# Optimization experiments

Hardware: AMD Instinct MI355X
Metric: run time of the kernel (lower is better)

## Reference

```python
import jax, jax.numpy as jnp
import numpy as np

B, N, FIN, E, OUT, NH = 8, 1024, 128, 128, 128, 8
HD = E // NH  # head_dim = 16


def setup_inputs() -> dict:
    key = jax.random.key(0)
    ks = jax.random.split(key, 8)
    s = 0.05
    H = jax.random.normal(ks[0], (B, N, FIN), jnp.float32)
    # binary adjacency (sparse-ish graph), stored dense float as the module expects
    A = (jax.random.uniform(ks[1], (B, N, N)) < 0.05).astype(jnp.float32)
    W_lin = jax.random.normal(ks[2], (FIN, E), jnp.float32) * s
    b_lin = jnp.zeros((E,), jnp.float32)
    # nn.MultiheadAttention packed in-projection (q,k,v) and out-projection
    W_in = jax.random.normal(ks[3], (E, 3 * E), jnp.float32) * s
    b_in = jnp.zeros((3 * E,), jnp.float32)
    W_out = jax.random.normal(ks[4], (E, E), jnp.float32) * s
    b_out = jnp.zeros((E,), jnp.float32)
    W_fin = jax.random.normal(ks[5], (E, OUT), jnp.float32) * s
    b_fin = jnp.zeros((OUT,), jnp.float32)
    return dict(H=H, A=A, W_lin=W_lin, b_lin=b_lin, W_in=W_in, b_in=b_in,
                W_out=W_out, b_out=b_out, W_fin=W_fin, b_fin=b_fin)


def reference(H, A, W_lin, b_lin, W_in, b_in, W_out, b_out, W_fin, b_fin):
    # input projection: Linear(128, embed_dim)
    Hp = H @ W_lin + b_lin                                   # (B,N,E)
    # adjacency-gated attention weights: bmm -> LeakyReLU(0.2) -> *A -> softmax
    s = jnp.einsum('bnd,bmd->bnm', Hp, Hp)                   # (B,N,N)
    s = jnp.where(s >= 0, s, 0.2 * s)
    attn_w = jax.nn.softmax(s * A, axis=-1)                  # (B,N,N)
    # nn.MultiheadAttention self-attention with float attn_mask (ADDED to scores)
    qkv = Hp @ W_in + b_in                                   # (B,N,3E)
    q, k, v = jnp.split(qkv, 3, axis=-1)
    q = q.reshape(B, N, NH, HD)
    k = k.reshape(B, N, NH, HD)
    v = v.reshape(B, N, NH, HD)
    scores = jnp.einsum('bnhd,bmhd->bhnm', q, k) / np.sqrt(HD).astype(np.float32)
    scores = scores + attn_w[:, None]                        # mask broadcast over heads
    p = jax.nn.softmax(scores, axis=-1)                      # (B,NH,N,N)
    o = jnp.einsum('bhnm,bmhd->bnhd', p, v).reshape(B, N, E)
    o = o @ W_out + b_out                                    # MHA out_proj
    # output linear; dropout is identity in eval mode
    return o @ W_fin + b_fin                                 # (B,N,OUT)
```

## Files before the change

kernel.cpp:

```cpp
#include <hip/hip_runtime.h>
#include <hip/hip_bf16.h>


using u16 = unsigned short;
typedef short bf16x8 __attribute__((ext_vector_type(8)));
typedef float f32x4 __attribute__((ext_vector_type(4)));
typedef _Float16 f16;
typedef _Float16 f16x4 __attribute__((ext_vector_type(4)));

#define MFMA16(a, b, c) __builtin_amdgcn_mfma_f32_16x16x16f16(a, b, c, 0, 0, 0)

__device__ __forceinline__ u16 f2b(float f) {
    unsigned u = __float_as_uint(f);
    return (u16)((u + 0x7fffu + ((u >> 16) & 1u)) >> 16);
}
__device__ __forceinline__ float b2f(u16 u) {
    return __uint_as_float(((unsigned)u) << 16);
}

__global__ void prep_k(const float* __restrict__ Wlin, const float* __restrict__ Win,
                       const float* __restrict__ Wout, const float* __restrict__ Wfin,
                       const float* __restrict__ bout, const float* __restrict__ bfin,
                       const float* __restrict__ Aadj,
                       u16* __restrict__ WlinTb, u16* __restrict__ WinTb,
                       float* __restrict__ WcombT, float* __restrict__ bcomb,
                       float* __restrict__ rowsum, unsigned char* __restrict__ A8) {
    int i = blockIdx.x * 256 + threadIdx.x;
    if (i >= 81920) {
        int j = i - 81920;
        long long base = (long long)j * 8;
        float4 a0 = *(const float4*)&Aadj[base];
        float4 a1 = *(const float4*)&Aadj[base + 4];
        unsigned long long m = 0;
        m |= (unsigned long long)(a0.x != 0.f) << 0;
        m |= (unsigned long long)(a0.y != 0.f) << 8;
        m |= (unsigned long long)(a0.z != 0.f) << 16;
        m |= (unsigned long long)(a0.w != 0.f) << 24;
        m |= (unsigned long long)(a1.x != 0.f) << 32;
        m |= (unsigned long long)(a1.y != 0.f) << 40;
        m |= (unsigned long long)(a1.z != 0.f) << 48;
        m |= (unsigned long long)(a1.w != 0.f) << 56;
        *(unsigned long long*)&A8[base] = m;
        return;
    }
    if (i < 8192) rowsum[i] = 0.f;
    if (i < 16384) {
        WlinTb[(i & 127) * 128 + (i >> 7)] = f2b(Wlin[i]);
    } else if (i < 65536) {
        int k = i - 16384;
        int r = k / 384, c = k - r * 384;
        WinTb[c * 128 + r] = f2b(Win[k]);
    } else {
        int k = i - 65536;
        int o = k & 127, e = k >> 7;
        float s = 0.f;
        for (int kk = 0; kk < 128; ++kk)
            s = fmaf(Wout[e * 128 + kk], Wfin[kk * 128 + o], s);
        WcombT[o * 128 + e] = s;
        if (e == 0) {
            float sb = bfin[o];
            for (int kk = 0; kk < 128; ++kk)
                sb = fmaf(bout[kk], Wfin[kk * 128 + o], sb);
            bcomb[o] = sb;
        }
    }
}

__global__ __launch_bounds__(256)
void mfma_hp(const float* __restrict__ A, const u16* __restrict__ Bb,
             const float* __restrict__ bias, u16* __restrict__ C) {
    const int m0 = blockIdx.x * 128;
    const int t = threadIdx.x;
    const int wave = t >> 6, lane = t & 63;
    const int wm = (wave >> 1) * 64, wn = (wave & 1) * 64;
    const int m16 = lane & 15, kq = lane >> 4;
    f32x4 acc[4][4] = {};

#pragma unroll
    for (int kc = 0; kc < 4; ++kc) {
        bf16x8 af[4], bf[4];
#pragma unroll
        for (int i = 0; i < 4; ++i) {
            const float* ap = &A[(long long)(m0 + wm + i * 16 + m16) * 128 + kc * 32 + kq * 8];
            float4 u0 = *(const float4*)ap;
            float4 u1 = *(const float4*)(ap + 4);
            bf16x8 a;
            a[0] = (short)f2b(u0.x); a[1] = (short)f2b(u0.y);
            a[2] = (short)f2b(u0.z); a[3] = (short)f2b(u0.w);
            a[4] = (short)f2b(u1.x); a[5] = (short)f2b(u1.y);
            a[6] = (short)f2b(u1.z); a[7] = (short)f2b(u1.w);
            af[i] = a;
        }
#pragma unroll
        for (int j = 0; j < 4; ++j)
            bf[j] = *(const bf16x8*)&Bb[(long long)(wn + j * 16 + m16) * 128 + kc * 32 + kq * 8];
#pragma unroll
        for (int i = 0; i < 4; ++i)
#pragma unroll
            for (int j = 0; j < 4; ++j)
                acc[i][j] = __builtin_amdgcn_mfma_f32_16x16x32_bf16(af[i], bf[j], acc[i][j], 0, 0, 0);
    }
#pragma unroll
    for (int i = 0; i < 4; ++i) {
#pragma unroll
        for (int r = 0; r < 4; ++r) {
            long long row = m0 + wm + i * 16 + kq * 4 + r;
#pragma unroll
            for (int j = 0; j < 4; ++j) {
                int col = wn + j * 16 + m16;
                C[row * 128 + col] = f2b(acc[i][j][r] + bias[col]);
            }
        }
    }
}

__global__ __launch_bounds__(256)
void mfma_qkvz(const u16* __restrict__ Hpb, const u16* __restrict__ WinTb,
               const float* __restrict__ bin, f16* __restrict__ Cq,
               const unsigned char* __restrict__ G8, u16* __restrict__ EZ,
               float* __restrict__ rowsum) {
    const int blk = blockIdx.x;
    const int t = threadIdx.x;
    const int wave = t >> 6, lane = t & 63;
    const int wm = (wave >> 1) * 64, wn = (wave & 1) * 64;
    const int m16 = lane & 15, kq = lane >> 4;
    f32x4 acc[4][4] = {};

    if (blk < 512) {
        const int b = blk >> 6, mt = (blk >> 3) & 7, nt = blk & 7;
        const u16* Ab = Hpb + (long long)b * 1024 * 128;
        const int m0 = mt * 128, n0 = nt * 128;
#pragma unroll
        for (int kc = 0; kc < 4; ++kc) {
            bf16x8 af[4], bf[4];
#pragma unroll
            for (int i = 0; i < 4; ++i)
                af[i] = *(const bf16x8*)&Ab[(long long)(m0 + wm + i * 16 + m16) * 128 + kc * 32 + kq * 8];
#pragma unroll
            for (int j = 0; j < 4; ++j)
                bf[j] = *(const bf16x8*)&Ab[(long long)(n0 + wn + j * 16 + m16) * 128 + kc * 32 + kq * 8];
#pragma unroll
            for (int i = 0; i < 4; ++i)
#pragma unroll
                for (int j = 0; j < 4; ++j)
                    acc[i][j] = __builtin_amdgcn_mfma_f32_16x16x32_bf16(af[i], bf[j], acc[i][j], 0, 0, 0);
        }
        const long long zb = (long long)b * 1024 * 1024;
#pragma unroll
        for (int i = 0; i < 4; ++i) {
#pragma unroll
            for (int r = 0; r < 4; ++r) {
                int row = m0 + wm + i * 16 + kq * 4 + r;
                float es = 0.f;
#pragma unroll
                for (int j = 0; j < 4; ++j) {
                    int col = n0 + wn + j * 16 + m16;
                    float v = acc[i][j][r];
                    v = v >= 0.f ? v : 0.2f * v;
                    if (!G8[zb + (long long)row * 1024 + col]) v = 0.f;
                    float ev = __expf(v);
                    EZ[zb + (long long)row * 1024 + col] = f2b(ev);
                    es += ev;
                }
#pragma unroll
                for (int off = 1; off < 16; off <<= 1) es += __shfl_xor(es, off);
                if (m16 == 0) atomicAdd(&rowsum[b * 1024 + row], es);
            }
        }
    } else {
        const int q = blk - 512;
        const int mt = q & 63, slab = q >> 6;
        const int m0 = mt * 128;
        const u16* Bslab = WinTb + (long long)slab * 128 * 128;
#pragma unroll
        for (int kc = 0; kc < 4; ++kc) {
            bf16x8 af[4], bf[4];
#pragma unroll
            for (int i = 0; i < 4; ++i)
                af[i] = *(const bf16x8*)&Hpb[(long long)(m0 + wm + i * 16 + m16) * 128 + kc * 32 + kq * 8];
#pragma unroll
            for (int j = 0; j < 4; ++j)
                bf[j] = *(const bf16x8*)&Bslab[(long long)(wn + j * 16 + m16) * 128 + kc * 32 + kq * 8];
#pragma unroll
            for (int i = 0; i < 4; ++i)
#pragma unroll
                for (int j = 0; j < 4; ++j)
                    acc[i][j] = __builtin_amdgcn_mfma_f32_16x16x32_bf16(af[i], bf[j], acc[i][j], 0, 0, 0);
        }
        const float qscale = (slab == 0) ? 0.25f : 1.f;
#pragma unroll
        for (int i = 0; i < 4; ++i) {
#pragma unroll
            for (int r = 0; r < 4; ++r) {
                long long row = m0 + wm + i * 16 + kq * 4 + r;
#pragma unroll
                for (int j = 0; j < 4; ++j) {
                    int col = wn + j * 16 + m16;
                    float v = (acc[i][j][r] + bin[slab * 128 + col]) * qscale;
                    Cq[row * 384 + slab * 128 + col] = (f16)v;
                }
            }
        }
    }
}

__global__ __launch_bounds__(256)
void flash_mfma(const f16* __restrict__ qkv, const u16* __restrict__ ez,
                const float* __restrict__ rowsum, float* __restrict__ o_) {
    const int n0 = blockIdx.x * 64;
    const int b = blockIdx.y;
    const int h0 = blockIdx.z * 2;
    const int t = threadIdx.x;
    const int w = t >> 6, lane = t & 63;
    const int qr16 = lane & 15, quad = lane >> 4;

    __shared__ u16 Ks[64 * 40];
    __shared__ u16 VTs[32 * 76];
    __shared__ u16 AWs[64 * 72];

    const int qrow_l = w * 16 + qr16;
    const long long qrow_g = b * 1024 + n0 + qrow_l;
    const float inv0 = 1.f / rowsum[qrow_g];

    f16x4 qf[2];
#pragma unroll
    for (int hh = 0; hh < 2; ++hh)
        qf[hh] = *(const f16x4*)&qkv[qrow_g * 384 + (h0 + hh) * 16 + quad * 4];

    f32x4 accO[2] = {};
    float lacc[2] = {0.f, 0.f};

    for (int st = 0; st < 16; ++st) {
        const int kb = st * 64;
        __syncthreads();
        {
            const int key = t >> 2, c8 = t & 3;
            *(uint4*)&Ks[key * 40 + c8 * 8] =
                *(const uint4*)&qkv[((long long)(b * 1024 + kb + key)) * 384 + 128 + h0 * 16 + c8 * 8];
            const f16* vsrc = &qkv[((long long)(b * 1024 + kb + key)) * 384 + 256 + h0 * 16 + c8 * 8];
            f16x4 v0 = *(const f16x4*)vsrc;
            f16x4 v1 = *(const f16x4*)(vsrc + 4);
            const int d0 = c8 * 8;
#pragma unroll
            for (int i = 0; i < 4; ++i) {
                VTs[(d0 + i) * 76 + key] = ((const u16*)&v0)[i];
                VTs[(d0 + 4 + i) * 76 + key] = ((const u16*)&v1)[i];
            }
        }
#pragma unroll
        for (int rr = 0; rr < 2; ++rr) {
            int idx = rr * 256 + t;
            int row = idx >> 3, c16 = idx & 7;
            *(uint4*)&AWs[row * 72 + c16 * 8] =
                *(const uint4*)&ez[((long long)(b * 1024 + n0 + row)) * 1024 + kb + c16 * 8];
        }
        __syncthreads();

#pragma unroll 2
        for (int kt = 0; kt < 4; ++kt) {
            ushort4 ue = *(const ushort4*)&AWs[qrow_l * 72 + kt * 16 + quad * 4];
            f32x4 aw0;
            aw0[0] = b2f(ue.x) * inv0; aw0[1] = b2f(ue.y) * inv0;
            aw0[2] = b2f(ue.z) * inv0; aw0[3] = b2f(ue.w) * inv0;
#pragma unroll
            for (int hh = 0; hh < 2; ++hh) {
                f16x4 kf = *(const f16x4*)&Ks[(kt * 16 + qr16) * 40 + hh * 16 + quad * 4];
                f32x4 s4 = MFMA16(kf, qf[hh], aw0);
                float p0 = __expf(s4[0]), p1 = __expf(s4[1]);
                float p2 = __expf(s4[2]), p3 = __expf(s4[3]);
                lacc[hh] += (p0 + p1) + (p2 + p3);
                f16x4 pf;
                pf[0] = (f16)p0; pf[1] = (f16)p1; pf[2] = (f16)p2; pf[3] = (f16)p3;
                f16x4 vf = *(const f16x4*)&VTs[(hh * 16 + qr16) * 76 + kt * 16 + quad * 4];
                accO[hh] = MFMA16(vf, pf, accO[hh]);
            }
        }
    }
#pragma unroll
    for (int hh = 0; hh < 2; ++hh) {
        float l = lacc[hh];
        l += __shfl_xor(l, 16);
        l += __shfl_xor(l, 32);
        float inv = 1.f / l;
        float* orow = o_ + qrow_g * 128 + (h0 + hh) * 16 + quad * 4;
#pragma unroll
        for (int r = 0; r < 4; ++r) orow[r] = accO[hh][r] * inv;
    }
}

__global__ __launch_bounds__(256)
void out_fused(const float* __restrict__ o_, const float* __restrict__ Bm,
               const float* __restrict__ bias, float* __restrict__ C) {
    const int m0 = blockIdx.x * 64, n0 = blockIdx.y * 64;
    __shared__ float As[64][132];
    __shared__ float Bs[64][68];
    const int t = threadIdx.x;
    const int tx = t & 15, ty = t >> 4;

#pragma unroll
    for (int g = 0; g < 8; ++g) {
        int flat = g * 256 + t;
        int row = flat >> 5;
        int d0 = (flat & 31) * 4;
        *(float4*)&As[row][d0] = *(const float4*)&o_[(long long)(m0 + row) * 128 + d0];
    }

    float acc[4][4] = {};
    for (int kt = 0; kt < 128; kt += 64) {
        __syncthreads();
#pragma unroll
        for (int r = 0; r < 4; ++r) {
            int flat = r * 256 + t;
            int row = flat >> 4;
            int k0 = (flat & 15) * 4;
            *(float4*)&Bs[row][k0] = *(const float4*)&Bm[(long long)(n0 + row) * 128 + kt + k0];
        }
        __syncthreads();
#pragma unroll
        for (int kc = 0; kc < 16; ++kc) {
            float4 a4[4], b4[4];
#pragma unroll
            for (int i = 0; i < 4; ++i) a4[i] = *(float4*)&As[16 * i + ty][kt + kc * 4];
#pragma unroll
            for (int j = 0; j < 4; ++j) b4[j] = *(float4*)&Bs[16 * j + tx][kc * 4];
#pragma unroll
            for (int i = 0; i < 4; ++i)
#pragma unroll
                for (int j = 0; j < 4; ++j) {
                    float s = acc[i][j];
                    s = fmaf(a4[i].x, b4[j].x, s);
                    s = fmaf(a4[i].y, b4[j].y, s);
                    s = fmaf(a4[i].z, b4[j].z, s);
                    s = fmaf(a4[i].w, b4[j].w, s);
                    acc[i][j] = s;
                }
        }
    }
#pragma unroll
    for (int i = 0; i < 4; ++i) {
        int row = m0 + 16 * i + ty;
#pragma unroll
        for (int j = 0; j < 4; ++j) {
            int col = n0 + 16 * j + tx;
            C[(long long)row * 128 + col] = acc[i][j] + bias[col];
        }
    }
}

extern "C" void kernel_launch(void* const* d_in, const int* in_sizes, int n_in,
                              void* d_out, int out_size, void* d_ws, size_t ws_size,
                              hipStream_t stream) {
    (void)in_sizes; (void)n_in; (void)out_size; (void)ws_size;
    const float* H    = (const float*)d_in[0];
    const float* Aadj = (const float*)d_in[1];
    const float* Wlin = (const float*)d_in[2];
    const float* blin = (const float*)d_in[3];
    const float* Win  = (const float*)d_in[4];
    const float* bin  = (const float*)d_in[5];
    const float* Wout = (const float*)d_in[6];
    const float* bout = (const float*)d_in[7];
    const float* Wfin = (const float*)d_in[8];
    const float* bfin = (const float*)d_in[9];
    float* out = (float*)d_out;
    char* ws = (char*)d_ws;

    u16*   WlinTb = (u16*)(ws + 0);
    u16*   WinTb  = (u16*)(ws + 32768);
    float* WcombT = (float*)(ws + 131072);
    float* bcomb  = (float*)(ws + 196608);
    float* rowsum = (float*)(ws + 197120);
    u16*   Hpb    = (u16*)(ws + 262144);
    f16*   qkv    = (f16*)(ws + 2359296);
    float* o_     = (float*)(ws + 8650752);
    u16*   ez     = (u16*)(ws + 12845056);
    unsigned char* A8 = (unsigned char*)(ws + 29622272);

    prep_k<<<4416, 256, 0, stream>>>(Wlin, Win, Wout, Wfin, bout, bfin, Aadj,
                                     WlinTb, WinTb, WcombT, bcomb, rowsum, A8);
    mfma_hp<<<64, 256, 0, stream>>>(H, WlinTb, blin, Hpb);
    mfma_qkvz<<<704, 256, 0, stream>>>(Hpb, WinTb, bin, qkv, A8, ez, rowsum);
    flash_mfma<<<dim3(16, 8, 4), 256, 0, stream>>>(qkv, ez, rowsum, o_);
    out_fused<<<dim3(128, 2), 256, 0, stream>>>(o_, WcombT, bcomb, out);
}
```

Before: 170.0 us.

## Fuse input projection into prep kernel and switch output GEMM to bf16 MFMA

Merges the Hp = H·W_lin MFMA GEMM into the prep kernel as 64 extra blocks that read W_lin directly with strided fp32 loads, which drops one kernel launch and the transposed W_lin copy. The combined W_out·W_fin matrix is now stored as bf16, and the final projection uses an MFMA bf16 GEMM in place of the fp32 shared-memory FMA kernel. The cost is uncoalesced W_lin reads inside the fused blocks and extra bf16 rounding on the output path.

```diff
diff --git a/kernel.cpp b/kernel.cpp
--- a/kernel.cpp
+++ b/kernel.cpp
@@ -18,14 +18,68 @@
     return __uint_as_float(((unsigned)u) << 16);
 }
 
-__global__ void prep_k(const float* __restrict__ Wlin, const float* __restrict__ Win,
-                       const float* __restrict__ Wout, const float* __restrict__ Wfin,
-                       const float* __restrict__ bout, const float* __restrict__ bfin,
-                       const float* __restrict__ Aadj,
-                       u16* __restrict__ WlinTb, u16* __restrict__ WinTb,
-                       float* __restrict__ WcombT, float* __restrict__ bcomb,
-                       float* __restrict__ rowsum, unsigned char* __restrict__ A8) {
-    int i = blockIdx.x * 256 + threadIdx.x;
+__global__ void prep_hp(const float* __restrict__ H, const float* __restrict__ Wlin,
+                        const float* __restrict__ Win,
+                        const float* __restrict__ Wout, const float* __restrict__ Wfin,
+                        const float* __restrict__ bout, const float* __restrict__ bfin,
+                        const float* __restrict__ blin, const float* __restrict__ Aadj,
+                        u16* __restrict__ WinTb, u16* __restrict__ WcombTb,
+                        float* __restrict__ bcomb, float* __restrict__ rowsum,
+                        unsigned char* __restrict__ A8, u16* __restrict__ Hpb) {
+    if (blockIdx.x < 64) {
+        const int m0 = blockIdx.x * 128;
+        const int t = threadIdx.x;
+        const int wave = t >> 6, lane = t & 63;
+        const int wm = (wave >> 1) * 64, wn = (wave & 1) * 64;
+        const int m16 = lane & 15, kq = lane >> 4;
+        f32x4 acc[4][4] = {};
+
+#pragma unroll
+        for (int kc = 0; kc < 4; ++kc) {
+            bf16x8 af[4], bf[4];
+#pragma unroll
+            for (int i = 0; i < 4; ++i) {
+                const float* ap = &H[(long long)(m0 + wm + i * 16 + m16) * 128 + kc * 32 + kq * 8];
+                float4 u0 = *(const float4*)ap;
+                float4 u1 = *(const float4*)(ap + 4);
+                bf16x8 a;
+                a[0] = (short)f2b(u0.x); a[1] = (short)f2b(u0.y);
+                a[2] = (short)f2b(u0.z); a[3] = (short)f2b(u0.w);
+                a[4] = (short)f2b(u1.x); a[5] = (short)f2b(u1.y);
+                a[6] = (short)f2b(u1.z); a[7] = (short)f2b(u1.w);
+                af[i] = a;
+            }
+#pragma unroll
+            for (int j = 0; j < 4; ++j) {
+                const int col = wn + j * 16 + m16;
+                const int k0 = kc * 32 + kq * 8;
+                bf16x8 bb;
+#pragma unroll
+                for (int e = 0; e < 8; ++e)
+                    bb[e] = (short)f2b(Wlin[(long long)(k0 + e) * 128 + col]);
+                bf[j] = bb;
+            }
+#pragma unroll
+            for (int i = 0; i < 4; ++i)
+#pragma unroll
+                for (int j = 0; j < 4; ++j)
+                    acc[i][j] = __builtin_amdgcn_mfma_f32_16x16x32_bf16(af[i], bf[j], acc[i][j], 0, 0, 0);
+        }
+#pragma unroll
+        for (int i = 0; i < 4; ++i) {
+#pragma unroll
+            for (int r = 0; r < 4; ++r) {
+                long long row = m0 + wm + i * 16 + kq * 4 + r;
+#pragma unroll
+                for (int j = 0; j < 4; ++j) {
+                    int col = wn + j * 16 + m16;
+                    Hpb[row * 128 + col] = f2b(acc[i][j][r] + blin[col]);
+                }
+            }
+        }
+        return;
+    }
+    int i = (blockIdx.x - 64) * 256 + threadIdx.x;
     if (i >= 81920) {
         int j = i - 81920;
         long long base = (long long)j * 8;
@@ -44,72 +98,22 @@
         return;
     }
     if (i < 8192) rowsum[i] = 0.f;
-    if (i < 16384) {
-        WlinTb[(i & 127) * 128 + (i >> 7)] = f2b(Wlin[i]);
-    } else if (i < 65536) {
+    if (i >= 16384 && i < 65536) {
         int k = i - 16384;
         int r = k / 384, c = k - r * 384;
         WinTb[c * 128 + r] = f2b(Win[k]);
-    } else {
+    } else if (i >= 65536) {
         int k = i - 65536;
         int o = k & 127, e = k >> 7;
         float s = 0.f;
         for (int kk = 0; kk < 128; ++kk)
             s = fmaf(Wout[e * 128 + kk], Wfin[kk * 128 + o], s);
-        WcombT[o * 128 + e] = s;
+        WcombTb[o * 128 + e] = f2b(s);
         if (e == 0) {
             float sb = bfin[o];
             for (int kk = 0; kk < 128; ++kk)
                 sb = fmaf(bout[kk], Wfin[kk * 128 + o], sb);
             bcomb[o] = sb;
-        }
-    }
-}
-
-__global__ __launch_bounds__(256)
-void mfma_hp(const float* __restrict__ A, const u16* __restrict__ Bb,
-             const float* __restrict__ bias, u16* __restrict__ C) {
-    const int m0 = blockIdx.x * 128;
-    const int t = threadIdx.x;
-    const int wave = t >> 6, lane = t & 63;
-    const int wm = (wave >> 1) * 64, wn = (wave & 1) * 64;
-    const int m16 = lane & 15, kq = lane >> 4;
-    f32x4 acc[4][4] = {};
-
-#pragma unroll
-    for (int kc = 0; kc < 4; ++kc) {
-        bf16x8 af[4], bf[4];
-#pragma unroll
-        for (int i = 0; i < 4; ++i) {
-            const float* ap = &A[(long long)(m0 + wm + i * 16 + m16) * 128 + kc * 32 + kq * 8];
-            float4 u0 = *(const float4*)ap;
-            float4 u1 = *(const float4*)(ap + 4);
-            bf16x8 a;
-            a[0] = (short)f2b(u0.x); a[1] = (short)f2b(u0.y);
-            a[2] = (short)f2b(u0.z); a[3] = (short)f2b(u0.w);
-            a[4] = (short)f2b(u1.x); a[5] = (short)f2b(u1.y);
-            a[6] = (short)f2b(u1.z); a[7] = (short)f2b(u1.w);
-            af[i] = a;
-        }
-#pragma unroll
-        for (int j = 0; j < 4; ++j)
-            bf[j] = *(const bf16x8*)&Bb[(long long)(wn + j * 16 + m16) * 128 + kc * 32 + kq * 8];
-#pragma unroll
-        for (int i = 0; i < 4; ++i)
-#pragma unroll
-            for (int j = 0; j < 4; ++j)
-                acc[i][j] = __builtin_amdgcn_mfma_f32_16x16x32_bf16(af[i], bf[j], acc[i][j], 0, 0, 0);
-    }
-#pragma unroll
-    for (int i = 0; i < 4; ++i) {
-#pragma unroll
-        for (int r = 0; r < 4; ++r) {
-            long long row = m0 + wm + i * 16 + kq * 4 + r;
-#pragma unroll
-            for (int j = 0; j < 4; ++j) {
-                int col = wn + j * 16 + m16;
-                C[row * 128 + col] = f2b(acc[i][j][r] + bias[col]);
-            }
         }
     }
 }
@@ -289,60 +293,49 @@
 }
 
 __global__ __launch_bounds__(256)
-void out_fused(const float* __restrict__ o_, const float* __restrict__ Bm,
-               const float* __restrict__ bias, float* __restrict__ C) {
-    const int m0 = blockIdx.x * 64, n0 = blockIdx.y * 64;
-    __shared__ float As[64][132];
-    __shared__ float Bs[64][68];
+void mfma_out(const float* __restrict__ A, const u16* __restrict__ Bb,
+              const float* __restrict__ bias, float* __restrict__ C) {
+    const int m0 = blockIdx.x * 128;
     const int t = threadIdx.x;
-    const int tx = t & 15, ty = t >> 4;
-
-#pragma unroll
-    for (int g = 0; g < 8; ++g) {
-        int flat = g * 256 + t;
-        int row = flat >> 5;
-        int d0 = (flat & 31) * 4;
-        *(float4*)&As[row][d0] = *(const float4*)&o_[(long long)(m0 + row) * 128 + d0];
-    }
-
-    float acc[4][4] = {};
-    for (int kt = 0; kt < 128; kt += 64) {
-        __syncthreads();
+    const int wave = t >> 6, lane = t & 63;
+    const int wm = (wave >> 1) * 64, wn = (wave & 1) * 64;
+    const int m16 = lane & 15, kq = lane >> 4;
+    f32x4 acc[4][4] = {};
+
+#pragma unroll
+    for (int kc = 0; kc < 4; ++kc) {
+        bf16x8 af[4], bf[4];
+#pragma unroll
+        for (int i = 0; i < 4; ++i) {
+            const float* ap = &A[(long long)(m0 + wm + i * 16 + m16) * 128 + kc * 32 + kq * 8];
+            float4 u0 = *(const float4*)ap;
+            float4 u1 = *(const float4*)(ap + 4);
+            bf16x8 a;
+            a[0] = (short)f2b(u0.x); a[1] = (short)f2b(u0.y);
+            a[2] = (short)f2b(u0.z); a[3] = (short)f2b(u0.w);
+            a[4] = (short)f2b(u1.x); a[5] = (short)f2b(u1.y);
+            a[6] = (short)f2b(u1.z); a[7] = (short)f2b(u1.w);
+            af[i] = a;
+        }
+#pragma unroll
+        for (int j = 0; j < 4; ++j)
+            bf[j] = *(const bf16x8*)&Bb[(long long)(wn + j * 16 + m16) * 128 + kc * 32 + kq * 8];
+#pragma unroll
+        for (int i = 0; i < 4; ++i)
+#pragma unroll
+            for (int j = 0; j < 4; ++j)
+                acc[i][j] = __builtin_amdgcn_mfma_f32_16x16x32_bf16(af[i], bf[j], acc[i][j], 0, 0, 0);
+    }
+#pragma unroll
+    for (int i = 0; i < 4; ++i) {
 #pragma unroll
         for (int r = 0; r < 4; ++r) {
-            int flat = r * 256 + t;
-            int row = flat >> 4;
-            int k0 = (flat & 15) * 4;
-            *(float4*)&Bs[row][k0] = *(const float4*)&Bm[(long long)(n0 + row) * 128 + kt + k0];
-        }
-        __syncthreads();
-#pragma unroll
-        for (int kc = 0; kc < 16; ++kc) {
-            float4 a4[4], b4[4];
-#pragma unroll
-            for (int i = 0; i < 4; ++i) a4[i] = *(float4*)&As[16 * i + ty][kt + kc * 4];
-#pragma unroll
-            for (int j = 0; j < 4; ++j) b4[j] = *(float4*)&Bs[16 * j + tx][kc * 4];
-#pragma unroll
-            for (int i = 0; i < 4; ++i)
-#pragma unroll
-                for (int j = 0; j < 4; ++j) {
-                    float s = acc[i][j];
-                    s = fmaf(a4[i].x, b4[j].x, s);
-                    s = fmaf(a4[i].y, b4[j].y, s);
-                    s = fmaf(a4[i].z, b4[j].z, s);
-                    s = fmaf(a4[i].w, b4[j].w, s);
-                    acc[i][j] = s;
-                }
-        }
-    }
-#pragma unroll
-    for (int i = 0; i < 4; ++i) {
-        int row = m0 + 16 * i + ty;
-#pragma unroll
-        for (int j = 0; j < 4; ++j) {
-            int col = n0 + 16 * j + tx;
-            C[(long long)row * 128 + col] = acc[i][j] + bias[col];
+            long long row = m0 + wm + i * 16 + kq * 4 + r;
+#pragma unroll
+            for (int j = 0; j < 4; ++j) {
+                int col = wn + j * 16 + m16;
+                C[row * 128 + col] = acc[i][j][r] + bias[col];
+            }
         }
     }
 }
@@ -364,21 +357,20 @@
     float* out = (float*)d_out;
     char* ws = (char*)d_ws;
 
-    u16*   WlinTb = (u16*)(ws + 0);
-    u16*   WinTb  = (u16*)(ws + 32768);
-    float* WcombT = (float*)(ws + 131072);
-    float* bcomb  = (float*)(ws + 196608);
-    float* rowsum = (float*)(ws + 197120);
-    u16*   Hpb    = (u16*)(ws + 262144);
-    f16*   qkv    = (f16*)(ws + 2359296);
-    float* o_     = (float*)(ws + 8650752);
-    u16*   ez     = (u16*)(ws + 12845056);
+    u16*   WinTb   = (u16*)(ws + 0);
+    u16*   WcombTb = (u16*)(ws + 98304);
+    float* bcomb   = (float*)(ws + 131072);
+    float* rowsum  = (float*)(ws + 131584);
+    u16*   Hpb     = (u16*)(ws + 262144);
+    f16*   qkv     = (f16*)(ws + 2359296);
+    float* o_      = (float*)(ws + 8650752);
+    u16*   ez      = (u16*)(ws + 12845056);
     unsigned char* A8 = (unsigned char*)(ws + 29622272);
 
-    prep_k<<<4416, 256, 0, stream>>>(Wlin, Win, Wout, Wfin, bout, bfin, Aadj,
-                                     WlinTb, WinTb, WcombT, bcomb, rowsum, A8);
-    mfma_hp<<<64, 256, 0, stream>>>(H, WlinTb, blin, Hpb);
+    prep_hp<<<4480, 256, 0, stream>>>(H, Wlin, Win, Wout, Wfin, bout, bfin,
+                                      blin, Aadj, WinTb, WcombTb, bcomb,
+                                      rowsum, A8, Hpb);
     mfma_qkvz<<<704, 256, 0, stream>>>(Hpb, WinTb, bin, qkv, A8, ez, rowsum);
     flash_mfma<<<dim3(16, 8, 4), 256, 0, stream>>>(qkv, ez, rowsum, o_);
-    out_fused<<<dim3(128, 2), 256, 0, stream>>>(o_, WcombT, bcomb, out);
-}
+    mfma_out<<<64, 256, 0, stream>>>(o_, WcombTb, bcomb, out);
+}
```

New measurement: 163.0 us, median of 2. 4.1% less time.
